# Optimization experiments

Hardware: AMD Instinct MI355X
Metric: run time of the kernel (lower is better)

## Reference

```python
import jax, jax.numpy as jnp
import numpy as np

B, S, HID = 2, 2048, 2048
N_HEADS, HEAD_DIM = 16, 128
SCALE = 1.0 / np.sqrt(HEAD_DIM)
SOFTCAP = 30.0
WINDOW = 1024


def setup_inputs() -> dict:
    key = jax.random.key(0)
    ks = jax.random.split(key, 5)
    w_std = 1.0 / np.sqrt(HID)
    return {
        "x": jax.random.normal(ks[0], (B, S, HID), dtype=jnp.float32),
        "Wq": jax.random.normal(ks[1], (HID, HID), dtype=jnp.float32) * w_std,
        "Wk": jax.random.normal(ks[2], (HID, HID), dtype=jnp.float32) * w_std,
        "Wv": jax.random.normal(ks[3], (HID, HID), dtype=jnp.float32) * w_std,
        "Wo": jax.random.normal(ks[4], (HID, HID), dtype=jnp.float32) * w_std,
    }


def reference(x, Wq, Wk, Wv, Wo):
    b, s, _ = x.shape
    # fused-style QKV projections (nn.Linear: y = x @ W.T), split into heads
    def proj(W):
        y = jnp.einsum('bsh,oh->bso', x, W)
        return y.reshape(b, s, N_HEADS, HEAD_DIM).transpose(0, 2, 1, 3)  # [B,H,S,D]
    q, k, v = proj(Wq), proj(Wk), proj(Wv)

    scores = jnp.einsum('bhsd,bhtd->bhst', q, k) * SCALE  # [B,H,S,S]
    # logit soft-capping: softcap * tanh(logits / softcap)
    scores = SOFTCAP * jnp.tanh(scores / SOFTCAP)

    # causal + sliding-window mask: attend to j in (i - WINDOW, i]
    i = jnp.arange(s)[:, None]
    j = jnp.arange(s)[None, :]
    allowed = (j <= i) & ((i - j) < WINDOW)
    scores = jnp.where(allowed, scores, jnp.finfo(scores.dtype).min)

    p = jax.nn.softmax(scores, axis=-1)
    attn = jnp.einsum('bhst,bhtd->bhsd', p, v)  # [B,H,S,D]
    attn = attn.transpose(0, 2, 1, 3).reshape(b, s, HID)
    out = jnp.einsum('bsh,oh->bso', attn, Wo)
    return out
```

## Files before the change

kernel.cpp:

```cpp
#include <hip/hip_runtime.h>

#define B_SZ 2
#define S_LEN 2048
#define HID_DIM 2048
#define NHEADS 16
#define HEAD_D 128
#define WIN 1024
#define M_ROWS (B_SZ * S_LEN)
#define NXC 8388608

typedef __attribute__((ext_vector_type(8))) short bf16x8;
typedef __attribute__((ext_vector_type(4))) float f32x4;

#define SCALE_F 0.08838834764831845f
#define SOFTCAP_F 30.0f

__device__ __forceinline__ unsigned short f2bf(float f) {
  unsigned u = __builtin_bit_cast(unsigned, f);
  unsigned r = (u + 0x7FFFu + ((u >> 16) & 1u)) >> 16;
  return (unsigned short)r;
}

__device__ __forceinline__ void vmwait5() { asm volatile("s_waitcnt vmcnt(5)" ::: "memory"); }
__device__ __forceinline__ void vmwait6() { asm volatile("s_waitcnt vmcnt(6)" ::: "memory"); }
__device__ __forceinline__ void vmwait0() { asm volatile("s_waitcnt vmcnt(0)" ::: "memory"); }
__device__ __forceinline__ void pbar()    { asm volatile("s_barrier" ::: "memory"); }

__global__ __launch_bounds__(256)
void cvt_all_kernel(const float* __restrict__ x,  const float* __restrict__ Wq,
                    const float* __restrict__ Wk, const float* __restrict__ Wv,
                    const float* __restrict__ Wo, unsigned short* __restrict__ dst) {
  const int i = blockIdx.x * 256 + threadIdx.x;
  const int a0 = 1048576;
  const int aw = 524288;
  const float* src;
  float scale = 1.0f;
  int j = i;
  if (i < a0) { src = x; }
  else if (i < a0 + aw)     { src = Wq; j = i - a0;          scale = SCALE_F / SOFTCAP_F; }
  else if (i < a0 + 2 * aw) { src = Wk; j = i - a0 - aw; }
  else if (i < a0 + 3 * aw) { src = Wv; j = i - a0 - 2 * aw; }
  else                      { src = Wo; j = i - a0 - 3 * aw; }
  const f32x4* p = (const f32x4*)src + (size_t)j * 2;
  f32x4 a = p[0], b = p[1];
  bf16x8 o;
  o[0] = (short)f2bf(a[0] * scale); o[1] = (short)f2bf(a[1] * scale);
  o[2] = (short)f2bf(a[2] * scale); o[3] = (short)f2bf(a[3] * scale);
  o[4] = (short)f2bf(b[0] * scale); o[5] = (short)f2bf(b[1] * scale);
  o[6] = (short)f2bf(b[2] * scale); o[7] = (short)f2bf(b[3] * scale);
  *((bf16x8*)dst + i) = o;
}

__device__ __forceinline__ void gload16(const unsigned short* g, unsigned short* l) {
  __builtin_amdgcn_global_load_lds(
      (const __attribute__((address_space(1))) unsigned int*)g,
      (__attribute__((address_space(3))) unsigned int*)l, 16, 0, 0);
}

__global__ __launch_bounds__(512, 2)
void gemm_qkv_kernel(const unsigned short* __restrict__ A,
                     const unsigned short* __restrict__ Bm,
                     unsigned short* __restrict__ Out) {
  extern __shared__ char smem[];
  constexpr int K = 2048, NT = 64;
  constexpr int SLOTW = 20480;
  const int t = threadIdx.x;
  const int w = t >> 6, l = t & 63, c = l & 15, g = l >> 4;
  const int wr = w >> 2, wc = w & 3;
  const int xcd = blockIdx.x & 7, i = blockIdx.x >> 3;
  const int nt = xcd * 2 + (i & 1), mt = i >> 1;
  const int m0 = mt * 256, n0 = nt * 384;
  const unsigned short* Ab = A + (size_t)m0 * K;
  const unsigned short* Bb = Bm + (size_t)n0 * K;

  int aoff[2], boff[3];
#pragma unroll
  for (int j = 0; j < 2; ++j) {
    int S = j * 512 + t, rp = S >> 3, slu = (S & 7) ^ (rp & 7);
    aoff[j] = (rp * 2 + (slu >> 2)) * K + (slu & 3) * 8;
  }
#pragma unroll
  for (int j = 0; j < 3; ++j) {
    int S = j * 512 + t, rp = S >> 3, slu = (S & 7) ^ (rp & 7);
    boff[j] = (rp * 2 + (slu >> 2)) * K + (slu & 3) * 8;
  }
  auto sbase = [&](int s) { return (unsigned short*)smem + s * SLOTW; };
  auto stA = [&](int tt, int s, int j) {
    gload16(Ab + aoff[j] + tt * 32, sbase(s) + (j * 512 + t) * 8);
  };
  auto stB = [&](int tt, int s, int j) {
    gload16(Bb + boff[j] + tt * 32, sbase(s) + 8192 + (j * 512 + t) * 8);
  };
  auto rix = [&](int row) {
    return (row >> 1) * 64 + (((((row & 1) << 2) | g) ^ ((row >> 1) & 7)) * 8);
  };

  f32x4 acc[8][6];
#pragma unroll
  for (int mi = 0; mi < 8; ++mi)
#pragma unroll
    for (int nf = 0; nf < 6; ++nf) acc[mi][nf] = (f32x4)0.0f;

  stA(0, 0, 0); stA(0, 0, 1); stB(0, 0, 0); stB(0, 0, 1); stB(0, 0, 2);
  stA(1, 1, 0); stA(1, 1, 1); stB(1, 1, 0); stB(1, 1, 1); stB(1, 1, 2);
  vmwait5();
  pbar();

#pragma unroll 1
  for (int tt = 0; tt < NT; ++tt) {
    const int s = tt & 3, ns = (tt + 2) & 3;
    const bool pre = (tt + 2) < NT;
    unsigned short* sA = sbase(s);
    unsigned short* sB = sA + 8192;

    bf16x8 af[8], bf[2];
#pragma unroll
    for (int mi = 0; mi < 8; ++mi) af[mi] = *(const bf16x8*)&sA[rix(wr * 128 + mi * 16 + c)];
#pragma unroll
    for (int nf = 0; nf < 2; ++nf) bf[nf] = *(const bf16x8*)&sB[rix(wc * 96 + nf * 16 + c)];
    if (pre) { stA(tt + 2, ns, 0); stA(tt + 2, ns, 1); }
    pbar();
    __builtin_amdgcn_s_setprio(1);
#pragma unroll
    for (int mi = 0; mi < 8; ++mi)
#pragma unroll
      for (int nf = 0; nf < 2; ++nf)
        acc[mi][nf] = __builtin_amdgcn_mfma_f32_16x16x32_bf16(af[mi], bf[nf], acc[mi][nf], 0, 0, 0);
    __builtin_amdgcn_s_setprio(0);
    pbar();

#pragma unroll
    for (int nf = 0; nf < 2; ++nf) bf[nf] = *(const bf16x8*)&sB[rix(wc * 96 + (2 + nf) * 16 + c)];
    if (pre) { stB(tt + 2, ns, 0); stB(tt + 2, ns, 1); }
    pbar();
    __builtin_amdgcn_s_setprio(1);
#pragma unroll
    for (int mi = 0; mi < 8; ++mi)
#pragma unroll
      for (int nf = 0; nf < 2; ++nf)
        acc[mi][2 + nf] = __builtin_amdgcn_mfma_f32_16x16x32_bf16(af[mi], bf[nf], acc[mi][2 + nf], 0, 0, 0);
    __builtin_amdgcn_s_setprio(0);
    pbar();

#pragma unroll
    for (int nf = 0; nf < 2; ++nf) bf[nf] = *(const bf16x8*)&sB[rix(wc * 96 + (4 + nf) * 16 + c)];
    if (pre) { stB(tt + 2, ns, 2); }
    pbar();
    __builtin_amdgcn_s_setprio(1);
#pragma unroll
    for (int mi = 0; mi < 8; ++mi)
#pragma unroll
      for (int nf = 0; nf < 2; ++nf)
        acc[mi][4 + nf] = __builtin_amdgcn_mfma_f32_16x16x32_bf16(af[mi], bf[nf], acc[mi][4 + nf], 0, 0, 0);
    __builtin_amdgcn_s_setprio(0);
    if (pre) vmwait5(); else vmwait0();
    pbar();
  }

#pragma unroll
  for (int mi = 0; mi < 8; ++mi)
#pragma unroll
    for (int nf = 0; nf < 6; ++nf)
#pragma unroll
      for (int r = 0; r < 4; ++r) {
        int row = m0 + wr * 128 + mi * 16 + g * 4 + r;
        int col = n0 + wc * 96 + nf * 16 + c;
        int which = col >> 11;
        Out[(size_t)which * NXC + (size_t)row * 2048 + (col & 2047)] = f2bf(acc[mi][nf][r]);
      }
}

__global__ __launch_bounds__(512, 2)
void gemm_wo_kernel(const unsigned short* __restrict__ A,
                    const unsigned short* __restrict__ Bm,
                    float* __restrict__ Out) {
  extern __shared__ char smem[];
  constexpr int K = 2048, NT = 32;
  constexpr int SLOT = 49152;
  const int t = threadIdx.x;
  const int w = t >> 6, l = t & 63, c = l & 15, g = l >> 4;
  const int wr = w >> 2, wc = w & 3;
  const int xcd = blockIdx.x & 7, q = blockIdx.x >> 3;
  const int mt = q, nt = xcd;
  const int m0 = mt * 128, n0 = nt * 256;
  const unsigned short* Ab = A + (size_t)m0 * K;
  const unsigned short* Bb = Bm + (size_t)n0 * K;

  auto lA = [&](int s) { return (unsigned short*)(smem + s * SLOT); };
  auto lB = [&](int s) { return (unsigned short*)(smem + s * SLOT + 16384); };
  auto stA = [&](int tt, int s, int j) {
    int chunk = j * 512 + t, row = chunk >> 3, ch = chunk & 7;
    gload16(Ab + (size_t)row * K + tt * 64 + ((ch ^ (row & 7)) * 8), lA(s) + chunk * 8);
  };
  auto stB = [&](int tt, int s, int j) {
    int chunk = j * 512 + t, row = chunk >> 3, ch = chunk & 7;
    gload16(Bb + (size_t)row * K + tt * 64 + ((ch ^ (row & 7)) * 8), lB(s) + chunk * 8);
  };
  auto rdA = [&](unsigned short* base, int mi, int kk) {
    int row = wr * 64 + mi * 16 + c;
    int ch = (kk * 4 + g) ^ (row & 7);
    return *(const bf16x8*)&base[row * 64 + ch * 8];
  };
  auto rdB = [&](unsigned short* base, int nf, int kk) {
    int row = wc * 64 + nf * 16 + c;
    int ch = (kk * 4 + g) ^ (row & 7);
    return *(const bf16x8*)&base[row * 64 + ch * 8];
  };

  f32x4 acc[4][4];
#pragma unroll
  for (int i = 0; i < 4; ++i)
#pragma unroll
    for (int j = 0; j < 4; ++j) acc[i][j] = (f32x4)0.0f;

  stA(0, 0, 0); stA(0, 0, 1);
  stB(0, 0, 0); stB(0, 0, 1); stB(0, 0, 2); stB(0, 0, 3);
  stA(1, 1, 0); stA(1, 1, 1);
  stB(1, 1, 0); stB(1, 1, 1); stB(1, 1, 2); stB(1, 1, 3);
  vmwait6();
  pbar();

#pragma unroll 1
  for (int tt = 0; tt < NT; ++tt) {
    const int s = tt % 3, ns = (tt + 2) % 3;
    unsigned short* sA = lA(s);
    unsigned short* sB = lB(s);
    const bool pre = (tt + 2) < NT;

    bf16x8 af[4][2], bfr[2][2];
#pragma unroll
    for (int mi = 0; mi < 4; ++mi)
#pragma unroll
      for (int kk = 0; kk < 2; ++kk) af[mi][kk] = rdA(sA, mi, kk);
#pragma unroll
    for (int ni = 0; ni < 2; ++ni)
#pragma unroll
      for (int kk = 0; kk < 2; ++kk) bfr[ni][kk] = rdB(sB, ni, kk);
    if (pre) { stA(tt + 2, ns, 0); stA(tt + 2, ns, 1); stB(tt + 2, ns, 0); }
    pbar();
    __builtin_amdgcn_s_setprio(1);
#pragma unroll
    for (int kk = 0; kk < 2; ++kk)
#pragma unroll
      for (int mi = 0; mi < 4; ++mi)
#pragma unroll
        for (int ni = 0; ni < 2; ++ni)
          acc[mi][ni] = __builtin_amdgcn_mfma_f32_16x16x32_bf16(af[mi][kk], bfr[ni][kk],
                                                                acc[mi][ni], 0, 0, 0);
    __builtin_amdgcn_s_setprio(0);
    pbar();

#pragma unroll
    for (int ni = 0; ni < 2; ++ni)
#pragma unroll
      for (int kk = 0; kk < 2; ++kk) bfr[ni][kk] = rdB(sB, 2 + ni, kk);
    if (pre) { stB(tt + 2, ns, 1); stB(tt + 2, ns, 2); stB(tt + 2, ns, 3); }
    pbar();
    __builtin_amdgcn_s_setprio(1);
#pragma unroll
    for (int kk = 0; kk < 2; ++kk)
#pragma unroll
      for (int mi = 0; mi < 4; ++mi)
#pragma unroll
        for (int ni = 0; ni < 2; ++ni)
          acc[mi][2 + ni] = __builtin_amdgcn_mfma_f32_16x16x32_bf16(af[mi][kk], bfr[ni][kk],
                                                                    acc[mi][2 + ni], 0, 0, 0);
    __builtin_amdgcn_s_setprio(0);
    if (pre) vmwait6(); else vmwait0();
    pbar();
  }

#pragma unroll
  for (int mi = 0; mi < 4; ++mi)
#pragma unroll
    for (int nf = 0; nf < 4; ++nf)
#pragma unroll
      for (int r = 0; r < 4; ++r) {
        int row = m0 + wr * 64 + mi * 16 + g * 4 + r;
        int col = n0 + wc * 64 + nf * 16 + c;
        Out[(size_t)row * 2048 + col] = acc[mi][nf][r];
      }
}

__global__ __launch_bounds__(256, 2)
void attn_kernel(const unsigned short* __restrict__ Qb,
                 const unsigned short* __restrict__ Kb,
                 const unsigned short* __restrict__ Vb,
                 unsigned short* __restrict__ Ob) {
  __shared__ unsigned short K_lds[64 * HEAD_D];
  __shared__ unsigned short V_lds[HEAD_D * 64];
  __shared__ unsigned short P_lds[4][32 * 64];

  const int t = threadIdx.x;
  const int w = t >> 6, l = t & 63;
  const int g = l >> 4, c = l & 15;

  const int bid = blockIdx.x;
  const int widx = (bid & 7) * 64 + (bid >> 3);
  const int bh = widx >> 4;
  const int q0 = (widx & 15) * 128;
  const int b = bh >> 4, h = bh & 15;
  const size_t base = (size_t)b * S_LEN * HID_DIM + (size_t)h * HEAD_D;
  const int qw = q0 + w * 32;

  bf16x8 qf[2][4];
#pragma unroll
  for (int qh = 0; qh < 2; ++qh) {
    const unsigned short* qp = Qb + base + (size_t)(qw + qh * 16 + c) * HID_DIM + g * 8;
#pragma unroll
    for (int dch = 0; dch < 4; ++dch) qf[qh][dch] = *(const bf16x8*)(qp + dch * 32);
  }

  f32x4 acc[2][8];
#pragma unroll
  for (int qh = 0; qh < 2; ++qh)
#pragma unroll
    for (int dc = 0; dc < 8; ++dc) acc[qh][dc] = (f32x4)0.0f;
  f32x4 asum[2];
  asum[0] = (f32x4)0.0f; asum[1] = (f32x4)0.0f;
  bf16x8 ones;
#pragma unroll
  for (int j = 0; j < 8; ++j) ones[j] = (short)0x3F80;

  int kstart = q0 - (WIN - 1);
  if (kstart < 0) kstart = 0;
  kstart &= ~63;
  const int kend = q0 + 127;

  const float C1 = -1.0f / 3.0f;
  const float CE = SOFTCAP_F * 1.4426950408889634f;

  for (int k0 = kstart; k0 <= kend; k0 += 64) {
#pragma unroll
    for (int i = 0; i < 4; ++i) {
      int li = i * 256 + t;
      int row = li >> 4, chs = li & 15;
      int ch = chs ^ (row & 7);
      gload16(Kb + base + (size_t)(k0 + row) * HID_DIM + ch * 8, &K_lds[li * 8]);
    }
    {
      int m4 = t >> 4, ch = t & 15;
      const unsigned short* vg = Vb + base + (size_t)(k0 + 4 * m4) * HID_DIM + ch * 8;
      bf16x8 v0 = *(const bf16x8*)vg;
      bf16x8 v1 = *(const bf16x8*)(vg + HID_DIM);
      bf16x8 v2 = *(const bf16x8*)(vg + 2 * HID_DIM);
      bf16x8 v3 = *(const bf16x8*)(vg + 3 * HID_DIM);
#pragma unroll
      for (int j = 0; j < 8; ++j) {
        int d = ch * 8 + j;
        int sw = (j ^ ch) & 7;
        int e = (d * 64 + 4 * m4) ^ (sw << 3);
        unsigned long long val =
            (unsigned long long)(unsigned short)v0[j] |
            ((unsigned long long)(unsigned short)v1[j] << 16) |
            ((unsigned long long)(unsigned short)v2[j] << 32) |
            ((unsigned long long)(unsigned short)v3[j] << 48);
        *(unsigned long long*)&V_lds[e] = val;
      }
    }
    __syncthreads();

    if (k0 <= qw + 31 && k0 + 63 >= qw - (WIN - 1)) {
      f32x4 sc[2][4];
#pragma unroll
      for (int qh = 0; qh < 2; ++qh)
#pragma unroll
        for (int kc = 0; kc < 4; ++kc) sc[qh][kc] = (f32x4)0.0f;
#pragma unroll
      for (int kc = 0; kc < 4; ++kc) {
#pragma unroll
        for (int dch = 0; dch < 4; ++dch) {
          int row = kc * 16 + c;
          int e = (row * HEAD_D + dch * 32 + g * 8) ^ ((row & 7) << 3);
          bf16x8 kf = *(const bf16x8*)&K_lds[e];
#pragma unroll
          for (int qh = 0; qh < 2; ++qh)
            sc[qh][kc] = __builtin_amdgcn_mfma_f32_16x16x32_bf16(kf, qf[qh][dch],
                                                                 sc[qh][kc], 0, 0, 0);
        }
      }
#pragma unroll
      for (int qh = 0; qh < 2; ++qh) {
        const int qwh = qw + qh * 16;
        const int i_g = qwh + c;
        const bool full = (k0 + 63 <= qwh) && (qwh + 15 - k0 < WIN);
        const int qq = qh * 16 + c;
#pragma unroll
        for (int kc = 0; kc < 4; ++kc) {
          unsigned u[4];
#pragma unroll
          for (int r = 0; r < 4; ++r) {
            float y = sc[qh][kc][r];
            float y2 = y * y;
            float tpoly = y * __builtin_fmaf(y2, C1, 1.0f);
            float pv = __builtin_amdgcn_exp2f(__builtin_fmaf(tpoly, CE, -CE));
            if (!full) {
              int j_g = k0 + kc * 16 + g * 4 + r;
              bool okm = (j_g <= i_g) && (i_g - j_g < WIN);
              pv = okm ? pv : 0.0f;
            }
            u[r] = __builtin_bit_cast(unsigned, pv);
          }
          unsigned w0 = (u[0] >> 16) | (u[1] & 0xFFFF0000u);
          unsigned w1 = (u[2] >> 16) | (u[3] & 0xFFFF0000u);
          int e = (qq * 64 + kc * 16 + g * 4) ^ ((qq & 7) << 3);
          *(unsigned long long*)&P_lds[w][e] =
              (unsigned long long)w0 | ((unsigned long long)w1 << 32);
        }
      }
      bf16x8 pa[2][2];
#pragma unroll
      for (int qh = 0; qh < 2; ++qh)
#pragma unroll
        for (int kb = 0; kb < 2; ++kb) {
          int row = qh * 16 + c;
          int e = (row * 64 + kb * 32 + g * 8) ^ ((row & 7) << 3);
          pa[qh][kb] = *(const bf16x8*)&P_lds[w][e];
        }
#pragma unroll
      for (int qh = 0; qh < 2; ++qh)
#pragma unroll
        for (int kb = 0; kb < 2; ++kb)
          asum[qh] = __builtin_amdgcn_mfma_f32_16x16x32_bf16(pa[qh][kb], ones,
                                                             asum[qh], 0, 0, 0);
#pragma unroll
      for (int dc = 0; dc < 8; ++dc) {
#pragma unroll
        for (int kb = 0; kb < 2; ++kb) {
          int d = dc * 16 + c;
          int sw = ((d & 7) ^ ((d >> 3) & 7)) & 7;
          int e = (d * 64 + kb * 32 + g * 8) ^ (sw << 3);
          bf16x8 vf = *(const bf16x8*)&V_lds[e];
#pragma unroll
          for (int qh = 0; qh < 2; ++qh)
            acc[qh][dc] = __builtin_amdgcn_mfma_f32_16x16x32_bf16(pa[qh][kb], vf,
                                                                  acc[qh][dc], 0, 0, 0);
        }
      }
    }
    __syncthreads();
  }

#pragma unroll
  for (int qh = 0; qh < 2; ++qh)
#pragma unroll
    for (int r = 0; r < 4; ++r) {
      float rinv = 1.0f / asum[qh][r];
#pragma unroll
      for (int dc = 0; dc < 8; ++dc) {
        int qq = qw + qh * 16 + g * 4 + r;
        float o = acc[qh][dc][r] * rinv;
        Ob[base + (size_t)qq * HID_DIM + dc * 16 + c] = f2bf(o);
      }
    }
}

extern "C" void kernel_launch(void* const* d_in, const int* in_sizes, int n_in,
                              void* d_out, int out_size, void* d_ws, size_t ws_size,
                              hipStream_t stream) {
  const float* x  = (const float*)d_in[0];
  const float* Wq = (const float*)d_in[1];
  const float* Wk = (const float*)d_in[2];
  const float* Wv = (const float*)d_in[3];
  const float* Wo = (const float*)d_in[4];

  const size_t NX = (size_t)M_ROWS * HID_DIM;
  const size_t NW = (size_t)HID_DIM * HID_DIM;

  unsigned short* xb  = (unsigned short*)d_ws;
  unsigned short* Wqb = xb + NX;
  unsigned short* Wkb = Wqb + NW;
  unsigned short* Wvb = Wkb + NW;
  unsigned short* Wob = Wvb + NW;
  unsigned short* Qb  = Wob + NW;
  unsigned short* Kb  = Qb + NX;
  unsigned short* Vb  = Kb + NX;
  unsigned short* Ab  = xb;

  cvt_all_kernel<<<dim3(12288), 256, 0, stream>>>(x, Wq, Wk, Wv, Wo, xb);

  gemm_qkv_kernel<<<dim3(256), 512, 163840, stream>>>(xb, Wqb, Qb);

  attn_kernel<<<dim3(512), 256, 0, stream>>>(Qb, Kb, Vb, Ab);

  gemm_wo_kernel<<<dim3(256), 512, 147456, stream>>>(Ab, Wob, (float*)d_out);
}
```

Baseline: 215.5 us.

## Retile QKV GEMM to 128x256 tiles with K=64 steps and triple buffering

The QKV projection GEMM moves from 256x384 output tiles with K=32 steps over a 4-slot buffer to 128x256 tiles with K=64 steps over a 3-slot buffer, apparently mirroring the Wo GEMM layout. The grid grows from 256 to 768 blocks, with blocks mapped to XCDs by N tile, and the LDS swizzle and fragment reads are rewritten for 64-wide rows. The aim is better load balance across CUs and fewer barriers per unit of K. The cost is lower arithmetic intensity per tile, so more global and LDS traffic per FLOP.

```diff
diff --git a/kernel.cpp b/kernel.cpp
--- a/kernel.cpp
+++ b/kernel.cpp
@@ -21,7 +21,6 @@
   return (unsigned short)r;
 }
 
-__device__ __forceinline__ void vmwait5() { asm volatile("s_waitcnt vmcnt(5)" ::: "memory"); }
 __device__ __forceinline__ void vmwait6() { asm volatile("s_waitcnt vmcnt(6)" ::: "memory"); }
 __device__ __forceinline__ void vmwait0() { asm volatile("s_waitcnt vmcnt(0)" ::: "memory"); }
 __device__ __forceinline__ void pbar()    { asm volatile("s_barrier" ::: "memory"); }
@@ -62,109 +61,110 @@
                      const unsigned short* __restrict__ Bm,
                      unsigned short* __restrict__ Out) {
   extern __shared__ char smem[];
-  constexpr int K = 2048, NT = 64;
-  constexpr int SLOTW = 20480;
+  constexpr int K = 2048, NT = 32;
+  constexpr int SLOT = 49152;
   const int t = threadIdx.x;
   const int w = t >> 6, l = t & 63, c = l & 15, g = l >> 4;
   const int wr = w >> 2, wc = w & 3;
-  const int xcd = blockIdx.x & 7, i = blockIdx.x >> 3;
-  const int nt = xcd * 2 + (i & 1), mt = i >> 1;
-  const int m0 = mt * 256, n0 = nt * 384;
+  const int xcd = blockIdx.x & 7, q = blockIdx.x >> 3;
+  const int mt = q & 31, ntl = q >> 5;
+  const int nt = xcd * 3 + ntl;
+  const int m0 = mt * 128, n0 = nt * 256;
   const unsigned short* Ab = A + (size_t)m0 * K;
   const unsigned short* Bb = Bm + (size_t)n0 * K;
 
-  int aoff[2], boff[3];
-#pragma unroll
-  for (int j = 0; j < 2; ++j) {
-    int S = j * 512 + t, rp = S >> 3, slu = (S & 7) ^ (rp & 7);
-    aoff[j] = (rp * 2 + (slu >> 2)) * K + (slu & 3) * 8;
-  }
-#pragma unroll
-  for (int j = 0; j < 3; ++j) {
-    int S = j * 512 + t, rp = S >> 3, slu = (S & 7) ^ (rp & 7);
-    boff[j] = (rp * 2 + (slu >> 2)) * K + (slu & 3) * 8;
-  }
-  auto sbase = [&](int s) { return (unsigned short*)smem + s * SLOTW; };
+  auto lA = [&](int s) { return (unsigned short*)(smem + s * SLOT); };
+  auto lB = [&](int s) { return (unsigned short*)(smem + s * SLOT + 16384); };
   auto stA = [&](int tt, int s, int j) {
-    gload16(Ab + aoff[j] + tt * 32, sbase(s) + (j * 512 + t) * 8);
+    int chunk = j * 512 + t, row = chunk >> 3, ch = chunk & 7;
+    gload16(Ab + (size_t)row * K + tt * 64 + ((ch ^ (row & 7)) * 8), lA(s) + chunk * 8);
   };
   auto stB = [&](int tt, int s, int j) {
-    gload16(Bb + boff[j] + tt * 32, sbase(s) + 8192 + (j * 512 + t) * 8);
-  };
-  auto rix = [&](int row) {
-    return (row >> 1) * 64 + (((((row & 1) << 2) | g) ^ ((row >> 1) & 7)) * 8);
-  };
-
-  f32x4 acc[8][6];
-#pragma unroll
-  for (int mi = 0; mi < 8; ++mi)
-#pragma unroll
-    for (int nf = 0; nf < 6; ++nf) acc[mi][nf] = (f32x4)0.0f;
-
-  stA(0, 0, 0); stA(0, 0, 1); stB(0, 0, 0); stB(0, 0, 1); stB(0, 0, 2);
-  stA(1, 1, 0); stA(1, 1, 1); stB(1, 1, 0); stB(1, 1, 1); stB(1, 1, 2);
-  vmwait5();
+    int chunk = j * 512 + t, row = chunk >> 3, ch = chunk & 7;
+    gload16(Bb + (size_t)row * K + tt * 64 + ((ch ^ (row & 7)) * 8), lB(s) + chunk * 8);
+  };
+  auto rdA = [&](unsigned short* base, int mi, int kk) {
+    int row = wr * 64 + mi * 16 + c;
+    int ch = (kk * 4 + g) ^ (row & 7);
+    return *(const bf16x8*)&base[row * 64 + ch * 8];
+  };
+  auto rdB = [&](unsigned short* base, int nf, int kk) {
+    int row = wc * 64 + nf * 16 + c;
+    int ch = (kk * 4 + g) ^ (row & 7);
+    return *(const bf16x8*)&base[row * 64 + ch * 8];
+  };
+
+  f32x4 acc[4][4];
+#pragma unroll
+  for (int i = 0; i < 4; ++i)
+#pragma unroll
+    for (int j = 0; j < 4; ++j) acc[i][j] = (f32x4)0.0f;
+
+  stA(0, 0, 0); stA(0, 0, 1);
+  stB(0, 0, 0); stB(0, 0, 1); stB(0, 0, 2); stB(0, 0, 3);
+  stA(1, 1, 0); stA(1, 1, 1);
+  stB(1, 1, 0); stB(1, 1, 1); stB(1, 1, 2); stB(1, 1, 3);
+  vmwait6();
   pbar();
 
 #pragma unroll 1
   for (int tt = 0; tt < NT; ++tt) {
-    const int s = tt & 3, ns = (tt + 2) & 3;
+    const int s = tt % 3, ns = (tt + 2) % 3;
+    unsigned short* sA = lA(s);
+    unsigned short* sB = lB(s);
     const bool pre = (tt + 2) < NT;
-    unsigned short* sA = sbase(s);
-    unsigned short* sB = sA + 8192;
-
-    bf16x8 af[8], bf[2];
-#pragma unroll
-    for (int mi = 0; mi < 8; ++mi) af[mi] = *(const bf16x8*)&sA[rix(wr * 128 + mi * 16 + c)];
-#pragma unroll
-    for (int nf = 0; nf < 2; ++nf) bf[nf] = *(const bf16x8*)&sB[rix(wc * 96 + nf * 16 + c)];
-    if (pre) { stA(tt + 2, ns, 0); stA(tt + 2, ns, 1); }
+
+    bf16x8 af[4][2], bfr[2][2];
+#pragma unroll
+    for (int mi = 0; mi < 4; ++mi)
+#pragma unroll
+      for (int kk = 0; kk < 2; ++kk) af[mi][kk] = rdA(sA, mi, kk);
+#pragma unroll
+    for (int ni = 0; ni < 2; ++ni)
+#pragma unroll
+      for (int kk = 0; kk < 2; ++kk) bfr[ni][kk] = rdB(sB, ni, kk);
+    if (pre) { stA(tt + 2, ns, 0); stA(tt + 2, ns, 1); stB(tt + 2, ns, 0); }
     pbar();
     __builtin_amdgcn_s_setprio(1);
 #pragma unroll
-    for (int mi = 0; mi < 8; ++mi)
-#pragma unroll
-      for (int nf = 0; nf < 2; ++nf)
-        acc[mi][nf] = __builtin_amdgcn_mfma_f32_16x16x32_bf16(af[mi], bf[nf], acc[mi][nf], 0, 0, 0);
+    for (int kk = 0; kk < 2; ++kk)
+#pragma unroll
+      for (int mi = 0; mi < 4; ++mi)
+#pragma unroll
+        for (int ni = 0; ni < 2; ++ni)
+          acc[mi][ni] = __builtin_amdgcn_mfma_f32_16x16x32_bf16(af[mi][kk], bfr[ni][kk],
+                                                                acc[mi][ni], 0, 0, 0);
     __builtin_amdgcn_s_setprio(0);
     pbar();
 
 #pragma unroll
-    for (int nf = 0; nf < 2; ++nf) bf[nf] = *(const bf16x8*)&sB[rix(wc * 96 + (2 + nf) * 16 + c)];
-    if (pre) { stB(tt + 2, ns, 0); stB(tt + 2, ns, 1); }
+    for (int ni = 0; ni < 2; ++ni)
+#pragma unroll
+      for (int kk = 0; kk < 2; ++kk) bfr[ni][kk] = rdB(sB, 2 + ni, kk);
+    if (pre) { stB(tt + 2, ns, 1); stB(tt + 2, ns, 2); stB(tt + 2, ns, 3); }
     pbar();
     __builtin_amdgcn_s_setprio(1);
 #pragma unroll
-    for (int mi = 0; mi < 8; ++mi)
-#pragma unroll
-      for (int nf = 0; nf < 2; ++nf)
-        acc[mi][2 + nf] = __builtin_amdgcn_mfma_f32_16x16x32_bf16(af[mi], bf[nf], acc[mi][2 + nf], 0, 0, 0);
+    for (int kk = 0; kk < 2; ++kk)
+#pragma unroll
+      for (int mi = 0; mi < 4; ++mi)
+#pragma unroll
+        for (int ni = 0; ni < 2; ++ni)
+          acc[mi][2 + ni] = __builtin_amdgcn_mfma_f32_16x16x32_bf16(af[mi][kk], bfr[ni][kk],
+                                                                    acc[mi][2 + ni], 0, 0, 0);
     __builtin_amdgcn_s_setprio(0);
-    pbar();
-
-#pragma unroll
-    for (int nf = 0; nf < 2; ++nf) bf[nf] = *(const bf16x8*)&sB[rix(wc * 96 + (4 + nf) * 16 + c)];
-    if (pre) { stB(tt + 2, ns, 2); }
-    pbar();
-    __builtin_amdgcn_s_setprio(1);
-#pragma unroll
-    for (int mi = 0; mi < 8; ++mi)
-#pragma unroll
-      for (int nf = 0; nf < 2; ++nf)
-        acc[mi][4 + nf] = __builtin_amdgcn_mfma_f32_16x16x32_bf16(af[mi], bf[nf], acc[mi][4 + nf], 0, 0, 0);
-    __builtin_amdgcn_s_setprio(0);
-    if (pre) vmwait5(); else vmwait0();
+    if (pre) vmwait6(); else vmwait0();
     pbar();
   }
 
 #pragma unroll
-  for (int mi = 0; mi < 8; ++mi)
-#pragma unroll
-    for (int nf = 0; nf < 6; ++nf)
+  for (int mi = 0; mi < 4; ++mi)
+#pragma unroll
+    for (int nf = 0; nf < 4; ++nf)
 #pragma unroll
       for (int r = 0; r < 4; ++r) {
-        int row = m0 + wr * 128 + mi * 16 + g * 4 + r;
-        int col = n0 + wc * 96 + nf * 16 + c;
+        int row = m0 + wr * 64 + mi * 16 + g * 4 + r;
+        int col = n0 + wc * 64 + nf * 16 + c;
         int which = col >> 11;
         Out[(size_t)which * NXC + (size_t)row * 2048 + (col & 2047)] = f2bf(acc[mi][nf][r]);
       }
@@ -479,7 +479,7 @@
 
   cvt_all_kernel<<<dim3(12288), 256, 0, stream>>>(x, Wq, Wk, Wv, Wo, xb);
 
-  gemm_qkv_kernel<<<dim3(256), 512, 163840, stream>>>(xb, Wqb, Qb);
+  gemm_qkv_kernel<<<dim3(768), 512, 147456, stream>>>(xb, Wqb, Qb);
 
   attn_kernel<<<dim3(512), 256, 0, stream>>>(Qb, Kb, Vb, Ab);
 
```

Result: slower. 239.8 us (+11.3%).
